# Kernel tuning notes

Measured on AMD Instinct MI355X. Metric: run time of the kernel, lower is better.

Reference implementation:

```python
import jax, jax.numpy as jnp
import numpy as np

B, S, D, H = 2, 2048, 1024, 16
DH = D // H
SCALE = 1.0 / float(np.sqrt(DH))


def setup_inputs() -> dict:
    key = jax.random.key(0)
    ks = jax.random.split(key, 9)
    std = 1.0 / float(np.sqrt(D))
    x = jax.random.normal(ks[0], (B, S, D), dtype=jnp.float32)
    # causal mask: True = masked (future positions)
    mask = jnp.triu(jnp.ones((S, S), dtype=bool), k=1)
    Wq = jax.random.normal(ks[1], (D, D), dtype=jnp.float32) * std
    Wk = jax.random.normal(ks[2], (D, D), dtype=jnp.float32) * std
    Wv = jax.random.normal(ks[3], (D, D), dtype=jnp.float32) * std
    Wo = jax.random.normal(ks[4], (D, D), dtype=jnp.float32) * std
    bq = jax.random.normal(ks[5], (D,), dtype=jnp.float32) * 0.01
    bk = jax.random.normal(ks[6], (D,), dtype=jnp.float32) * 0.01
    bv = jax.random.normal(ks[7], (D,), dtype=jnp.float32) * 0.01
    bo = jax.random.normal(ks[8], (D,), dtype=jnp.float32) * 0.01
    return {"x": x, "mask": mask, "Wq": Wq, "bq": bq, "Wk": Wk, "bk": bk,
            "Wv": Wv, "bv": bv, "Wo": Wo, "bo": bo}


def _split_heads(t):
    # (B, S, D) -> (B, H, S, DH)
    return t.reshape(B, S, H, DH).transpose(0, 2, 1, 3)


def reference(x, mask, Wq, bq, Wk, bk, Wv, bv, Wo, bo):
    # torch nn.Linear: y = x @ W.T + b
    q = _split_heads(x @ Wq.T + bq)
    k = _split_heads(x @ Wk.T + bk)
    v = _split_heads(x @ Wv.T + bv)
    # scores: (B, H, S, S)
    scores = jnp.einsum('bhsd,bhtd->bhst', q, k) * SCALE
    scores = jnp.where(mask[None, None, :, :], jnp.float32(-1e9), scores)
    attn = jax.nn.softmax(scores, axis=-1)
    attn = jnp.nan_to_num(attn, nan=0.0)
    out = jnp.einsum('bhst,bhtd->bhsd', attn, v)
    out = out.transpose(0, 2, 1, 3).reshape(B, S, D)
    return out @ Wo.T + bo
```

## Files before the change

### kernel.cpp

```cpp
#include <hip/hip_runtime.h>

#define S_LEN  2048
#define DMODEL 1024
#define NHEAD  16
#define DHEAD  64
#define SCALE_F 0.125f
#define SL2E_F 0.180336880f

typedef unsigned short ushort_t;
typedef __attribute__((ext_vector_type(8))) short bf16x8;
typedef __attribute__((ext_vector_type(4))) float f32x4;

typedef __attribute__((address_space(1))) void gv_t;
typedef __attribute__((address_space(3))) void lv_t;

__device__ __forceinline__ ushort_t f2bf(float f) {
    unsigned u = __builtin_bit_cast(unsigned, f);
    unsigned r = (u + 0x7FFFu + ((u >> 16) & 1u)) >> 16;
    return (ushort_t)r;
}

__device__ __forceinline__ unsigned cvtpk_bf16(float a, float b) {
    unsigned r;
    asm("v_cvt_pk_bf16_f32 %0, %1, %2" : "=v"(r) : "v"(a), "v"(b));
    return r;
}

__device__ __forceinline__ void gload16(const ushort_t* g, ushort_t* l) {
    __builtin_amdgcn_global_load_lds((gv_t*)g, (lv_t*)l, 16, 0, 0);
}

template<int N> __device__ __forceinline__ void wait_vmcnt() {
    if constexpr (N == 8)      asm volatile("s_waitcnt vmcnt(8)" ::: "memory");
    else if constexpr (N == 6) asm volatile("s_waitcnt vmcnt(6)" ::: "memory");
    else if constexpr (N == 4) asm volatile("s_waitcnt vmcnt(4)" ::: "memory");
    else if constexpr (N == 3) asm volatile("s_waitcnt vmcnt(3)" ::: "memory");
    else                       asm volatile("s_waitcnt vmcnt(0)" ::: "memory");
}

__global__ void cast_all(const float* __restrict__ x,
                         const float* __restrict__ Wq, const float* __restrict__ Wk,
                         const float* __restrict__ Wv, const float* __restrict__ Wo,
                         ushort_t* __restrict__ dst, int n4) {
    int i = blockIdx.x * blockDim.x + threadIdx.x;
    int stride = gridDim.x * blockDim.x;
    for (int idx = i; idx < n4; idx += stride) {
        const float* src; int off;
        if (idx < 1048576)      { src = x;  off = idx; }
        else if (idx < 1310720) { src = Wq; off = idx - 1048576; }
        else if (idx < 1572864) { src = Wk; off = idx - 1310720; }
        else if (idx < 1835008) { src = Wv; off = idx - 1572864; }
        else                    { src = Wo; off = idx - 1835008; }
        float4 f = ((const float4*)src)[off];
        ushort4 o;
        o.x = f2bf(f.x); o.y = f2bf(f.y); o.z = f2bf(f.z); o.w = f2bf(f.w);
        ((ushort4*)dst)[idx] = o;
    }
}

template<int MODE, int BM>
__launch_bounds__(256)
__global__ void gemm_bt(const ushort_t* __restrict__ A, const ushort_t* __restrict__ Bw,
                        const float* __restrict__ b0, const float* __restrict__ b1,
                        const float* __restrict__ b2,
                        void* __restrict__ out0, void* __restrict__ out1, void* __restrict__ out2,
                        int M, int N, int K) {
    constexpr int MF = BM / 32;
    constexpr int NLOADS = BM / 64 + 2;
    __shared__ ushort_t As[3][BM][32];
    __shared__ ushort_t Bs[3][128][32];
    const int tid  = threadIdx.x;
    const int lane = tid & 63;
    const int w    = tid >> 6;
    const int wr   = w >> 1, wc = w & 1;
    const int m0   = blockIdx.x * BM;
    const int n0   = blockIdx.y * 128;
    const int l15  = lane & 15;
    const int lg   = lane >> 4;
    const int srow = lane >> 2;
    const int scol = ((lane & 3) ^ ((lane >> 3) & 3)) * 8;
    const int ck   = (l15 >> 1) & 3;

    f32x4 acc[MF][4] = {};

    auto stage = [&](int sbuf, int k0) {
#pragma unroll
        for (int j = 0; j < BM / 64; j++) {
            const int rg = (w * (BM / 64) + j) * 16;
            gload16(A + (size_t)(m0 + rg + srow) * K + k0 + scol, &As[sbuf][rg][0]);
        }
#pragma unroll
        for (int j = 0; j < 2; j++) {
            const int rg = (w * 2 + j) * 16;
            gload16(Bw + (size_t)(n0 + rg + srow) * K + k0 + scol, &Bs[sbuf][rg][0]);
        }
    };

    const int nt = K >> 5;
    stage(0, 0);
    stage(1, 32);
    int bcur = 0;

    for (int t = 0; t < nt; ++t) {
        if (t + 2 < nt) {
            int bst = bcur + 2; if (bst >= 3) bst -= 3;
            stage(bst, (t + 2) << 5);
            wait_vmcnt<2 * NLOADS>();
        } else if (t + 1 < nt) {
            wait_vmcnt<NLOADS>();
        } else {
            wait_vmcnt<0>();
        }
        __builtin_amdgcn_s_barrier();
        __builtin_amdgcn_sched_barrier(0);

        bf16x8 af[MF], bfr[4];
#pragma unroll
        for (int i = 0; i < MF; i++)
            af[i]  = *(const bf16x8*)&As[bcur][wr*(BM/2) + i*16 + l15][(lg ^ ck) * 8];
#pragma unroll
        for (int i = 0; i < 4;  i++)
            bfr[i] = *(const bf16x8*)&Bs[bcur][wc*64 + i*16 + l15][(lg ^ ck) * 8];

        __builtin_amdgcn_s_setprio(1);
#pragma unroll
        for (int mf = 0; mf < MF; mf++)
#pragma unroll
            for (int nf = 0; nf < 4; nf++)
                acc[mf][nf] = __builtin_amdgcn_mfma_f32_16x16x32_bf16(af[mf], bfr[nf], acc[mf][nf], 0, 0, 0);
        __builtin_amdgcn_s_setprio(0);

        asm volatile("s_waitcnt lgkmcnt(0)" ::: "memory");
        __builtin_amdgcn_sched_barrier(0);
        __builtin_amdgcn_s_barrier();
        bcur = (bcur == 2) ? 0 : bcur + 1;
    }

#pragma unroll
    for (int mf = 0; mf < MF; mf++) {
#pragma unroll
        for (int nf = 0; nf < 4; nf++) {
            const int col = n0 + wc*64 + nf*16 + l15;
            if constexpr (MODE == 2) {
                const float bv = b0[col];
#pragma unroll
                for (int r = 0; r < 4; r++) {
                    const int row = m0 + wr*(BM/2) + mf*16 + lg*4 + r;
                    ((float*)out0)[(size_t)row * N + col] = acc[mf][nf][r] + bv;
                }
            } else {
                const int mat = col >> 10;
                const int c   = col & 1023;
                const int h   = c >> 6, dh = c & 63;
                const float* bp = (mat == 0) ? b0 : ((mat == 1) ? b1 : b2);
                const float bv = bp[c];
#pragma unroll
                for (int r = 0; r < 4; r++) {
                    const int row = m0 + wr*(BM/2) + mf*16 + lg*4 + r;
                    const int b = row >> 11, s = row & 2047;
                    float v = acc[mf][nf][r] + bv;
                    if (mat == 0) {
                        v *= SL2E_F;
                        ((ushort_t*)out0)[((size_t)(b*NHEAD + h) * S_LEN + s) * DHEAD + dh] = f2bf(v);
                    } else if (mat == 1)
                        ((ushort_t*)out1)[((size_t)(b*NHEAD + h) * S_LEN + s) * DHEAD + dh] = f2bf(v);
                    else
                        ((ushort_t*)out2)[((size_t)(b*NHEAD + h) * DHEAD + dh) * S_LEN + s] = f2bf(v);
                }
            }
        }
    }
}

__launch_bounds__(256, 4)
__global__ void attn_fwd(const ushort_t* __restrict__ Q, const ushort_t* __restrict__ Kh,
                         const ushort_t* __restrict__ Vt, ushort_t* __restrict__ Aout) {
    __shared__ ushort_t Ks[2][64][64];
    __shared__ ushort_t Vs[2][64][64];
    __shared__ ushort_t Ps[4][16][64];
    const int tid  = threadIdx.x;
    const int lane = tid & 63;
    const int w    = tid >> 6;
    const int l15  = lane & 15, lg = lane >> 4;
    const int bh   = blockIdx.x;
    const int y    = blockIdx.y;
    const int kq   = y >> 3, g0 = y & 7;
    const int qt   = (kq == 0) ? 2*g0 : (kq == 1) ? (31 - 2*g0)
                   : (kq == 2) ? (2*g0 + 1) : (30 - 2*g0);

    const size_t qkbase = (size_t)bh * S_LEN * DHEAD;
    const size_t vtbase = (size_t)bh * DHEAD * S_LEN;

    const int rsub  = lane >> 3;
    const int csw   = ((lane & 7) ^ rsub) * 8;
    const int swz   = (l15 & 7) * 8;
    const int psxor = (l15 & 7) << 4;

    const int qw = qt * 64 + w * 16;

    bf16x8 aq[2];
#pragma unroll
    for (int kc = 0; kc < 2; kc++)
        aq[kc] = *(const bf16x8*)(Q + qkbase + (size_t)(qw + l15) * DHEAD + kc*32 + lg*8);

    float m = -3.0e38f, l = 0.0f;
    f32x4 o[4] = {};

    auto stage = [&](int buf, int t) {
        const int kv0 = t * 64;
        const ushort_t* kp = Kh + qkbase + (size_t)kv0 * DHEAD;
        const ushort_t* vp = Vt + vtbase + kv0;
#pragma unroll
        for (int j2 = 0; j2 < 2; j2++) {
            const int j  = w * 2 + j2;
            const int rg = j * 8 + rsub;
            gload16(kp + (size_t)rg * DHEAD + csw, &Ks[buf][j*8][0]);
            gload16(vp + (size_t)rg * S_LEN + csw, &Vs[buf][j*8][0]);
        }
    };

    ushort_t* psw = &Ps[w][0][0];
    char* psrow = (char*)(psw + l15 * 64);

    stage(0, 0);
    int buf = 0;

    for (int t = 0; t <= qt; t++) {
        if (t < qt) {
            stage(buf ^ 1, t + 1);
            wait_vmcnt<4>();
        } else {
            wait_vmcnt<0>();
        }
        __builtin_amdgcn_s_barrier();
        __builtin_amdgcn_sched_barrier(0);

        f32x4 sacc[4] = {};
        __builtin_amdgcn_s_setprio(1);
#pragma unroll
        for (int kc = 0; kc < 2; kc++)
#pragma unroll
            for (int nf = 0; nf < 4; nf++) {
                bf16x8 bk = *(const bf16x8*)&Ks[buf][nf*16 + l15][(kc*32 + lg*8) ^ swz];
                sacc[nf] = __builtin_amdgcn_mfma_f32_16x16x32_bf16(bk, aq[kc], sacc[nf], 0, 0, 0);
            }
        __builtin_amdgcn_s_setprio(0);

        if (t == qt) {
            const int rowq = qw + l15;
            const int kv0  = t * 64;
#pragma unroll
            for (int nf = 0; nf < 4; nf++)
#pragma unroll
                for (int r = 0; r < 4; r++) {
                    const int colk = kv0 + nf*16 + lg*4 + r;
                    if (colk > rowq) sacc[nf][r] = -3.0e38f;
                }
        }

        float mnf[4];
#pragma unroll
        for (int nf = 0; nf < 4; nf++)
            mnf[nf] = fmaxf(fmaxf(sacc[nf][0], sacc[nf][1]), fmaxf(sacc[nf][2], sacc[nf][3]));
        float mx = fmaxf(fmaxf(mnf[0], mnf[1]), fmaxf(mnf[2], mnf[3]));
        mx = fmaxf(mx, __shfl_xor(mx, 16));
        mx = fmaxf(mx, __shfl_xor(mx, 32));

        const bool skip = __all(mx <= m + 8.0f);
        const float mn = skip ? m : fmaxf(m, mx);

        float snf[4];
#pragma unroll
        for (int nf = 0; nf < 4; nf++) {
            const float p0 = exp2f(sacc[nf][0] - mn);
            const float p1 = exp2f(sacc[nf][1] - mn);
            const float p2 = exp2f(sacc[nf][2] - mn);
            const float p3 = exp2f(sacc[nf][3] - mn);
            uint2 pk;
            pk.x = cvtpk_bf16(p0, p1);
            pk.y = cvtpk_bf16(p2, p3);
            *(uint2*)(psrow + (((nf*16 + lg*4) * 2) ^ psxor)) = pk;
            snf[nf] = (p0 + p1) + (p2 + p3);
        }
        float s = (snf[0] + snf[1]) + (snf[2] + snf[3]);
        s += __shfl_xor(s, 16);
        s += __shfl_xor(s, 32);

        if (skip) {
            l += s;
        } else {
            const float corr = exp2f(m - mn);
            m = mn;
            l = l * corr + s;
            float cf[4];
#pragma unroll
            for (int r = 0; r < 4; r++) cf[r] = __shfl(corr, lg*4 + r);
#pragma unroll
            for (int nf = 0; nf < 4; nf++)
#pragma unroll
                for (int r = 0; r < 4; r++) o[nf][r] *= cf[r];
        }

        __builtin_amdgcn_s_setprio(1);
#pragma unroll
        for (int kc = 0; kc < 2; kc++) {
            bf16x8 pa = *(const bf16x8*)(psrow + (((kc*32 + lg*8) * 2) ^ psxor));
#pragma unroll
            for (int nf = 0; nf < 4; nf++) {
                bf16x8 bv = *(const bf16x8*)&Vs[buf][nf*16 + l15][(kc*32 + lg*8) ^ swz];
                o[nf] = __builtin_amdgcn_mfma_f32_16x16x32_bf16(pa, bv, o[nf], 0, 0, 0);
            }
        }
        __builtin_amdgcn_s_setprio(0);

        asm volatile("s_waitcnt lgkmcnt(0)" ::: "memory");
        __builtin_amdgcn_sched_barrier(0);
        __builtin_amdgcn_s_barrier();
        buf ^= 1;
    }

    const int b = bh >> 4, h = bh & 15;
    const float inv = 1.0f / l;
#pragma unroll
    for (int r = 0; r < 4; r++) {
        const float ia = __shfl(inv, lg*4 + r);
        const int rowq = qw + lg*4 + r;
#pragma unroll
        for (int nf = 0; nf < 4; nf++)
            Aout[((size_t)(b * S_LEN) + rowq) * DMODEL + h*DHEAD + nf*16 + l15] = f2bf(o[nf][r] * ia);
    }
}

extern "C" void kernel_launch(void* const* d_in, const int* in_sizes, int n_in,
                              void* d_out, int out_size, void* d_ws, size_t ws_size,
                              hipStream_t stream) {
    (void)in_sizes; (void)n_in; (void)out_size; (void)ws_size;
    const float* x  = (const float*)d_in[0];
    const float* Wq = (const float*)d_in[2];
    const float* bq = (const float*)d_in[3];
    const float* Wk = (const float*)d_in[4];
    const float* bk = (const float*)d_in[5];
    const float* Wv = (const float*)d_in[6];
    const float* bv = (const float*)d_in[7];
    const float* Wo = (const float*)d_in[8];
    const float* bo = (const float*)d_in[9];

    char* ws = (char*)d_ws;
    ushort_t* xb    = (ushort_t*)(ws);
    ushort_t* Wqkvb = (ushort_t*)(ws + (8u  << 20));
    ushort_t* Wob   = (ushort_t*)(ws + (14u << 20));
    ushort_t* Qh    = (ushort_t*)(ws + (16u << 20));
    ushort_t* Kh    = (ushort_t*)(ws + (24u << 20));
    ushort_t* Vth   = (ushort_t*)(ws + (32u << 20));
    ushort_t* Ao    = (ushort_t*)(ws + (40u << 20));

    cast_all<<<2048, 256, 0, stream>>>(x, Wq, Wk, Wv, Wo, xb, 2097152);

    gemm_bt<0, 128><<<dim3(32, 24), 256, 0, stream>>>(xb, Wqkvb, bq, bk, bv,
                                                      Qh, Kh, Vth, 2*S_LEN, 3*DMODEL, DMODEL);

    attn_fwd<<<dim3(2*NHEAD, 32), 256, 0, stream>>>(Qh, Kh, Vth, Ao);

    gemm_bt<2, 64><<<dim3(64, 8), 256, 0, stream>>>(Ao, Wob, bo, nullptr, nullptr,
                                                    d_out, nullptr, nullptr, 2*S_LEN, DMODEL, DMODEL);
}
```

Before: 115.7 us.

## Replace QKV projection GEMM with 256x256-tile, 512-thread pipelined kernel

Adds a dedicated QKV projection GEMM that uses 256x256 output tiles with 8 waves and BK=64. Operand staging is double-buffered, with global loads interleaved between MFMA quarter-steps and XOR-swizzled LDS. The larger tile is meant to raise operand reuse and cut global/LDS traffic per FLOP. The cost is only 192 blocks on a chip with 256 CUs, so some CUs sit idle, plus heavy register pressure and more barriers. The output GEMM is split into its own non-templated kernel, and the cast kernel gets a trivial index tweak.

New measurement: 144.3 us. 1.25x slower.

```diff
diff --git a/kernel.cpp b/kernel.cpp
--- a/kernel.cpp
+++ b/kernel.cpp
@@ -51,20 +51,201 @@
         else if (idx < 1572864) { src = Wk; off = idx - 1310720; }
         else if (idx < 1835008) { src = Wv; off = idx - 1572864; }
         else                    { src = Wo; off = idx - 1835008; }
-        float4 f = ((const float4*)src)[off];
+        float4 f = ((const float4*)src)[idx < 1048576 ? idx : off];
         ushort4 o;
         o.x = f2bf(f.x); o.y = f2bf(f.y); o.z = f2bf(f.z); o.w = f2bf(f.w);
         ((ushort4*)dst)[idx] = o;
     }
 }
 
-template<int MODE, int BM>
+__launch_bounds__(512, 1)
+__global__ void gemm_qkv(const ushort_t* __restrict__ A, const ushort_t* __restrict__ Bw,
+                         const float* __restrict__ b0, const float* __restrict__ b1,
+                         const float* __restrict__ b2,
+                         ushort_t* __restrict__ outQ, ushort_t* __restrict__ outK,
+                         ushort_t* __restrict__ outV) {
+    constexpr int K  = 1024;
+    constexpr int NT = 16;
+    __shared__ ushort_t As[2][256][64];
+    __shared__ ushort_t Bs[2][256][64];
+    const int tid  = threadIdx.x;
+    const int lane = tid & 63;
+    const int w    = tid >> 6;
+    const int wm   = w >> 2, wn = w & 3;
+    const int m0   = blockIdx.x * 256;
+    const int n0   = blockIdx.y * 256;
+    const int l15  = lane & 15;
+    const int lg   = lane >> 4;
+    const int r8   = lane >> 3;
+    const int c8   = ((lane & 7) ^ r8) * 8;
+    const int rck  = l15 & 7;
+
+    f32x4 acc[8][4] = {};
+    bf16x8 bfr[4][2];
+
+    auto stageA = [&](int tile, int half) {
+        const int k0 = tile * 64, buf = tile & 1;
+#pragma unroll
+        for (int j = 0; j < 2; j++) {
+            const int row = half * 128 + (w * 2 + j) * 8;
+            gload16(A + (size_t)(m0 + row + r8) * K + k0 + c8, &As[buf][row][0]);
+        }
+    };
+    auto stageB = [&](int tile, int half) {
+        const int k0 = tile * 64, buf = tile & 1;
+#pragma unroll
+        for (int j = 0; j < 2; j++) {
+            const int row = half * 128 + (w * 2 + j) * 8;
+            gload16(Bw + (size_t)(n0 + row + r8) * K + k0 + c8, &Bs[buf][row][0]);
+        }
+    };
+
+    stageA(0, 0); stageA(0, 1);
+    stageB(0, 0); stageB(0, 1);
+    stageB(1, 0); stageB(1, 1);
+
+    for (int i = 0; i < NT / 2; ++i) {
+        const int t0 = 2 * i, t1 = 2 * i + 1;
+
+        stageA(t1, 0);
+        wait_vmcnt<6>();
+        __builtin_amdgcn_s_barrier();
+        {
+#pragma unroll
+            for (int nf = 0; nf < 4; nf++)
+#pragma unroll
+                for (int kk = 0; kk < 2; kk++)
+                    bfr[nf][kk] = *(const bf16x8*)&Bs[0][wn*64 + nf*16 + l15][((kk*4 + lg) ^ rck) * 8];
+            bf16x8 af[2][2];
+#pragma unroll
+            for (int dm = 0; dm < 2; dm++)
+#pragma unroll
+                for (int kk = 0; kk < 2; kk++)
+                    af[dm][kk] = *(const bf16x8*)&As[0][wm*128 + dm*16 + l15][((kk*4 + lg) ^ rck) * 8];
+            __builtin_amdgcn_s_setprio(1);
+#pragma unroll
+            for (int kk = 0; kk < 2; kk++)
+#pragma unroll
+                for (int dm = 0; dm < 2; dm++)
+#pragma unroll
+                    for (int nf = 0; nf < 4; nf++)
+                        acc[dm][nf] = __builtin_amdgcn_mfma_f32_16x16x32_bf16(af[dm][kk], bfr[nf][kk], acc[dm][nf], 0, 0, 0);
+            __builtin_amdgcn_s_setprio(0);
+        }
+        __builtin_amdgcn_s_barrier();
+
+#pragma unroll
+        for (int q = 1; q < 4; q++) {
+            bf16x8 af[2][2];
+#pragma unroll
+            for (int dm = 0; dm < 2; dm++)
+#pragma unroll
+                for (int kk = 0; kk < 2; kk++)
+                    af[dm][kk] = *(const bf16x8*)&As[0][wm*128 + (q*2 + dm)*16 + l15][((kk*4 + lg) ^ rck) * 8];
+            if (q == 1)      stageA(t1, 1);
+            else if (q == 2) { if (t0 + 2 < NT) stageB(t0 + 2, 0); }
+            else             { if (t0 + 2 < NT) stageB(t0 + 2, 1); }
+            __builtin_amdgcn_s_barrier();
+            __builtin_amdgcn_s_setprio(1);
+#pragma unroll
+            for (int kk = 0; kk < 2; kk++)
+#pragma unroll
+                for (int dm = 0; dm < 2; dm++)
+#pragma unroll
+                    for (int nf = 0; nf < 4; nf++)
+                        acc[q*2 + dm][nf] = __builtin_amdgcn_mfma_f32_16x16x32_bf16(af[dm][kk], bfr[nf][kk], acc[q*2 + dm][nf], 0, 0, 0);
+            __builtin_amdgcn_s_setprio(0);
+            __builtin_amdgcn_s_barrier();
+        }
+
+        if (t0 + 2 < NT) {
+            stageA(t0 + 2, 0);
+            wait_vmcnt<6>();
+        } else {
+            wait_vmcnt<0>();
+        }
+        __builtin_amdgcn_s_barrier();
+        {
+#pragma unroll
+            for (int nf = 0; nf < 4; nf++)
+#pragma unroll
+                for (int kk = 0; kk < 2; kk++)
+                    bfr[nf][kk] = *(const bf16x8*)&Bs[1][wn*64 + nf*16 + l15][((kk*4 + lg) ^ rck) * 8];
+            bf16x8 af[2][2];
+#pragma unroll
+            for (int dm = 0; dm < 2; dm++)
+#pragma unroll
+                for (int kk = 0; kk < 2; kk++)
+                    af[dm][kk] = *(const bf16x8*)&As[1][wm*128 + dm*16 + l15][((kk*4 + lg) ^ rck) * 8];
+            __builtin_amdgcn_s_setprio(1);
+#pragma unroll
+            for (int kk = 0; kk < 2; kk++)
+#pragma unroll
+                for (int dm = 0; dm < 2; dm++)
+#pragma unroll
+                    for (int nf = 0; nf < 4; nf++)
+                        acc[dm][nf] = __builtin_amdgcn_mfma_f32_16x16x32_bf16(af[dm][kk], bfr[nf][kk], acc[dm][nf], 0, 0, 0);
+            __builtin_amdgcn_s_setprio(0);
+        }
+        __builtin_amdgcn_s_barrier();
+
+#pragma unroll
+        for (int q = 1; q < 4; q++) {
+            bf16x8 af[2][2];
+#pragma unroll
+            for (int dm = 0; dm < 2; dm++)
+#pragma unroll
+                for (int kk = 0; kk < 2; kk++)
+                    af[dm][kk] = *(const bf16x8*)&As[1][wm*128 + (q*2 + dm)*16 + l15][((kk*4 + lg) ^ rck) * 8];
+            if (q == 1)      { if (t0 + 2 < NT) stageA(t0 + 2, 1); }
+            else if (q == 2) { if (t1 + 2 < NT) stageB(t1 + 2, 0); }
+            else             { if (t1 + 2 < NT) stageB(t1 + 2, 1); }
+            __builtin_amdgcn_s_barrier();
+            __builtin_amdgcn_s_setprio(1);
+#pragma unroll
+            for (int kk = 0; kk < 2; kk++)
+#pragma unroll
+                for (int dm = 0; dm < 2; dm++)
+#pragma unroll
+                    for (int nf = 0; nf < 4; nf++)
+                        acc[q*2 + dm][nf] = __builtin_amdgcn_mfma_f32_16x16x32_bf16(af[dm][kk], bfr[nf][kk], acc[q*2 + dm][nf], 0, 0, 0);
+            __builtin_amdgcn_s_setprio(0);
+            __builtin_amdgcn_s_barrier();
+        }
+    }
+
+#pragma unroll
+    for (int mf = 0; mf < 8; mf++) {
+#pragma unroll
+        for (int nf = 0; nf < 4; nf++) {
+            const int col = n0 + wn*64 + nf*16 + l15;
+            const int mat = col >> 10;
+            const int c   = col & 1023;
+            const int h   = c >> 6, dh = c & 63;
+            const float* bp = (mat == 0) ? b0 : ((mat == 1) ? b1 : b2);
+            const float bv = bp[c];
+#pragma unroll
+            for (int r = 0; r < 4; r++) {
+                const int row = m0 + wm*128 + mf*16 + lg*4 + r;
+                const int b = row >> 11, s = row & 2047;
+                float v = acc[mf][nf][r] + bv;
+                if (mat == 0) {
+                    v *= SL2E_F;
+                    outQ[((size_t)(b*NHEAD + h) * S_LEN + s) * DHEAD + dh] = f2bf(v);
+                } else if (mat == 1)
+                    outK[((size_t)(b*NHEAD + h) * S_LEN + s) * DHEAD + dh] = f2bf(v);
+                else
+                    outV[((size_t)(b*NHEAD + h) * DHEAD + dh) * S_LEN + s] = f2bf(v);
+            }
+        }
+    }
+}
+
 __launch_bounds__(256)
-__global__ void gemm_bt(const ushort_t* __restrict__ A, const ushort_t* __restrict__ Bw,
-                        const float* __restrict__ b0, const float* __restrict__ b1,
-                        const float* __restrict__ b2,
-                        void* __restrict__ out0, void* __restrict__ out1, void* __restrict__ out2,
-                        int M, int N, int K) {
+__global__ void gemm_out(const ushort_t* __restrict__ A, const ushort_t* __restrict__ Bw,
+                         const float* __restrict__ b0, float* __restrict__ out0,
+                         int M, int N, int K) {
+    constexpr int BM = 64;
     constexpr int MF = BM / 32;
     constexpr int NLOADS = BM / 64 + 2;
     __shared__ ushort_t As[3][BM][32];
@@ -141,32 +322,11 @@
 #pragma unroll
         for (int nf = 0; nf < 4; nf++) {
             const int col = n0 + wc*64 + nf*16 + l15;
-            if constexpr (MODE == 2) {
-                const float bv = b0[col];
-#pragma unroll
-                for (int r = 0; r < 4; r++) {
-                    const int row = m0 + wr*(BM/2) + mf*16 + lg*4 + r;
-                    ((float*)out0)[(size_t)row * N + col] = acc[mf][nf][r] + bv;
-                }
-            } else {
-                const int mat = col >> 10;
-                const int c   = col & 1023;
-                const int h   = c >> 6, dh = c & 63;
-                const float* bp = (mat == 0) ? b0 : ((mat == 1) ? b1 : b2);
-                const float bv = bp[c];
-#pragma unroll
-                for (int r = 0; r < 4; r++) {
-                    const int row = m0 + wr*(BM/2) + mf*16 + lg*4 + r;
-                    const int b = row >> 11, s = row & 2047;
-                    float v = acc[mf][nf][r] + bv;
-                    if (mat == 0) {
-                        v *= SL2E_F;
-                        ((ushort_t*)out0)[((size_t)(b*NHEAD + h) * S_LEN + s) * DHEAD + dh] = f2bf(v);
-                    } else if (mat == 1)
-                        ((ushort_t*)out1)[((size_t)(b*NHEAD + h) * S_LEN + s) * DHEAD + dh] = f2bf(v);
-                    else
-                        ((ushort_t*)out2)[((size_t)(b*NHEAD + h) * DHEAD + dh) * S_LEN + s] = f2bf(v);
-                }
+            const float bv = b0[col];
+#pragma unroll
+            for (int r = 0; r < 4; r++) {
+                const int row = m0 + wr*(BM/2) + mf*16 + lg*4 + r;
+                out0[(size_t)row * N + col] = acc[mf][nf][r] + bv;
             }
         }
     }
@@ -356,11 +516,10 @@
 
     cast_all<<<2048, 256, 0, stream>>>(x, Wq, Wk, Wv, Wo, xb, 2097152);
 
-    gemm_bt<0, 128><<<dim3(32, 24), 256, 0, stream>>>(xb, Wqkvb, bq, bk, bv,
-                                                      Qh, Kh, Vth, 2*S_LEN, 3*DMODEL, DMODEL);
+    gemm_qkv<<<dim3(16, 12), 512, 0, stream>>>(xb, Wqkvb, bq, bk, bv, Qh, Kh, Vth);
 
     attn_fwd<<<dim3(2*NHEAD, 32), 256, 0, stream>>>(Qh, Kh, Vth, Ao);
 
-    gemm_bt<2, 64><<<dim3(64, 8), 256, 0, stream>>>(Ao, Wob, bo, nullptr, nullptr,
-                                                    d_out, nullptr, nullptr, 2*S_LEN, DMODEL, DMODEL);
-}
+    gemm_out<<<dim3(64, 8), 256, 0, stream>>>(Ao, Wob, bo, (float*)d_out,
+                                              2*S_LEN, DMODEL, DMODEL);
+}
```
